# Kernel optimization log

Measured on AMD Instinct MI355X. Metric: run time of the kernel, lower is better.

## Reference

```python
import jax, jax.numpy as jnp
import numpy as np

B, N, C = 2, 16384, 3        # clouds, points per cloud, feature dim
M, K = 2048, 64              # num_out_points (FPS centers), max_num_neighbors
R = 0.2                      # ball-query radius
H1, H2, HOUT = 64, 64, 128   # local_nn MLP widths


def setup_inputs() -> dict:
    key = jax.random.key(0)
    ks = jax.random.split(key, 8)
    return {
        "x": jax.random.normal(ks[0], (B, N, C), jnp.float32),
        "pos": jax.random.uniform(ks[1], (B, N, 3), jnp.float32),
        "W1": jax.random.normal(ks[2], (C + 3, H1), jnp.float32) * 0.1,
        "b1": jnp.zeros((H1,), jnp.float32),
        "W2": jax.random.normal(ks[3], (H1, H2), jnp.float32) * 0.1,
        "b2": jnp.zeros((H2,), jnp.float32),
        "W3": jax.random.normal(ks[4], (H2, HOUT), jnp.float32) * 0.1,
        "b3": jnp.zeros((HOUT,), jnp.float32),
    }


def _fps(pos):
    """Iterative farthest point sampling for one cloud. pos: [N,3] -> idx [M]."""
    mind = jnp.sum((pos - pos[0]) ** 2, axis=-1)  # start from point 0

    def step(mind, _):
        nxt = jnp.argmax(mind)
        mind = jnp.minimum(mind, jnp.sum((pos - pos[nxt]) ** 2, axis=-1))
        return mind, nxt.astype(jnp.int32)

    _, idx = jax.lax.scan(step, mind, None, length=M - 1)
    return jnp.concatenate([jnp.zeros((1,), jnp.int32), idx])


def reference(x, pos, W1, b1, W2, b2, W3, b3):
    # 1) FPS: pick M centers per cloud (vectorized over batch)
    idx = jax.vmap(_fps)(pos)                                   # [B, M]
    centers = jnp.take_along_axis(pos, idx[..., None], axis=1)  # [B, M, 3]

    # 2) ball query: up to K neighbors within radius R of each center
    d2 = jnp.sum((centers[:, :, None, :] - pos[:, None, :, :]) ** 2, axis=-1)  # [B,M,N]
    masked = jnp.where(d2 <= R * R, d2, jnp.inf)
    neg_top, nbr = jax.lax.top_k(-masked, K)   # K nearest within radius; nbr [B,M,K]
    valid = neg_top > -jnp.inf                 # in-radius mask

    # 3) gather -> local MLP -> max scatter (PointNetConv, aggr='max')
    gather = jax.vmap(lambda arr, i: arr[i])   # per-cloud fancy gather
    pos_j = gather(pos, nbr)                   # [B, M, K, 3]
    x_j = gather(x, nbr)                       # [B, M, K, C]
    rel = pos_j - centers[:, :, None, :]
    feat = jnp.concatenate([x_j, rel], axis=-1)          # [B, M, K, C+3]
    h = jax.nn.relu(feat @ W1 + b1)
    h = jax.nn.relu(h @ W2 + b2)
    h = h @ W3 + b3                                       # [B, M, K, HOUT]
    h = jnp.where(valid[..., None], h, -jnp.inf)
    out = jnp.max(h, axis=2)                              # [B, M, HOUT]
    out = jnp.where(jnp.isfinite(out), out, 0.0)          # empty-neighborhood guard
    return out, centers
```

## Files before the change

### kernel.cpp

```cpp
#include <hip/hip_runtime.h>
#include <cstdint>

#define NPT   16384
#define BATCH 2
#define MOUT  2048
#define KNBR  64
#define CAP   2048
#define FPS_T 1024
#define PPT   (NPT / FPS_T)
#define NW    (FPS_T / 64)

#define R2_F32 0.039999999105930328f

__device__ __forceinline__ float d2_exact(float ax, float ay, float az,
                                          float bx, float by, float bz) {
  float dx = __fsub_rn(ax, bx);
  float dy = __fsub_rn(ay, by);
  float dz = __fsub_rn(az, bz);
  return __fadd_rn(__fadd_rn(__fmul_rn(dx, dx), __fmul_rn(dy, dy)),
                   __fmul_rn(dz, dz));
}

template <int CTRL, int ROW>
__device__ __forceinline__ float dpp_max_step(float x) {
  int v = __float_as_int(x);
  int p = __builtin_amdgcn_update_dpp(v, v, CTRL, ROW, 0xF, false);
  return fmaxf(x, __int_as_float(p));
}

__device__ __forceinline__ float wave_max64(float x) {
  x = dpp_max_step<0xB1, 0xF>(x);
  x = dpp_max_step<0x4E, 0xF>(x);
  x = dpp_max_step<0x141, 0xF>(x);
  x = dpp_max_step<0x140, 0xF>(x);
  x = dpp_max_step<0x142, 0xA>(x);
  x = dpp_max_step<0x143, 0xC>(x);
  return __int_as_float(__builtin_amdgcn_readlane(__float_as_int(x), 63));
}

__global__ void prep_kernel(const float* __restrict__ W1,
                            const float* __restrict__ W2,
                            const float* __restrict__ W3,
                            float* __restrict__ ws) {
  int t = threadIdx.x + blockIdx.x * blockDim.x;
  int stride = blockDim.x * gridDim.x;
  for (int idx = t; idx < 64 * 6; idx += stride) {
    int j = idx / 6, i = idx - j * 6;
    ws[idx] = W1[i * 64 + j];
  }
  for (int idx = t; idx < 64 * 64; idx += stride) {
    int j = idx >> 6, i = idx & 63;
    ws[384 + idx] = W2[i * 64 + j];
  }
  for (int idx = t; idx < 128 * 64; idx += stride) {
    int j = idx >> 6, i = idx & 63;
    ws[4480 + idx] = W3[i * 128 + j];
  }
}

__device__ __forceinline__ int morton3_8(int x, int y, int z) {
  int c = 0;
#pragma unroll
  for (int k = 0; k < 3; ++k)
    c |= (((x >> k) & 1) << (3 * k)) | (((y >> k) & 1) << (3 * k + 1)) |
         (((z >> k) & 1) << (3 * k + 2));
  return c;
}

__global__ __launch_bounds__(512) void bin_kernel(
    const float* __restrict__ pos, float* __restrict__ sx,
    float* __restrict__ sy, float* __restrict__ sz, int* __restrict__ soi) {
  const int b = blockIdx.x;
  const int t = threadIdx.x;
  const float* __restrict__ P = pos + (size_t)b * NPT * 3;

  __shared__ int hist[512];
  __shared__ int scan[512];
  __shared__ unsigned short cid[NPT];

  hist[t] = 0;
  __syncthreads();

  for (int p = 0; p < 32; ++p) {
    int g = t + p * 512;
    float x = P[g * 3 + 0], y = P[g * 3 + 1], z = P[g * 3 + 2];
    int ix = (int)(x * 8.0f); ix = ix < 0 ? 0 : (ix > 7 ? 7 : ix);
    int iy = (int)(y * 8.0f); iy = iy < 0 ? 0 : (iy > 7 ? 7 : iy);
    int iz = (int)(z * 8.0f); iz = iz < 0 ? 0 : (iz > 7 ? 7 : iz);
    int c = morton3_8(ix, iy, iz);
    cid[g] = (unsigned short)c;
    atomicAdd(&hist[c], 1);
  }
  __syncthreads();

  int cnt = hist[t];
  int v = cnt;
  scan[t] = v;
  __syncthreads();
  for (int off = 1; off < 512; off <<= 1) {
    int add = (t >= off) ? scan[t - off] : 0;
    __syncthreads();
    v += add;
    scan[t] = v;
    __syncthreads();
  }
  hist[t] = scan[t] - cnt;
  __syncthreads();

  for (int p = 0; p < 32; ++p) {
    int g = t + p * 512;
    int c = cid[g];
    int dst = atomicAdd(&hist[c], 1);
    sx[b * NPT + dst] = P[g * 3 + 0];
    sy[b * NPT + dst] = P[g * 3 + 1];
    sz[b * NPT + dst] = P[g * 3 + 2];
    soi[b * NPT + dst] = g;
  }
}

__global__ __launch_bounds__(FPS_T, 4) void fps_kernel(
    const float* __restrict__ pos, const float* __restrict__ sx,
    const float* __restrict__ sy, const float* __restrict__ sz,
    const int* __restrict__ soi, float* __restrict__ centers) {
  const int b = blockIdx.x;
  const int t = threadIdx.x;
  const int lane = t & 63;
  const int wid = t >> 6;
  const float* __restrict__ P = pos + (size_t)b * NPT * 3;
  float* __restrict__ Cout = centers + (size_t)b * MOUT * 3;

  __shared__ int oidL[NPT];
  __shared__ float wmax[NW];
  __shared__ unsigned long long qpack[2][3];

  float px[PPT], py[PPT], pz[PPT], mind[PPT];
  const int base = b * NPT + t * PPT;
#pragma unroll
  for (int p = 0; p < PPT; ++p) {
    px[p] = sx[base + p];
    py[p] = sy[base + p];
    pz[p] = sz[base + p];
    oidL[t * PPT + p] = soi[base + p];
  }

  float lox = px[0], hix = px[0], loy = py[0], hiy = py[0], loz = pz[0], hiz = pz[0];
#pragma unroll
  for (int p = 1; p < PPT; ++p) {
    lox = fminf(lox, px[p]); hix = fmaxf(hix, px[p]);
    loy = fminf(loy, py[p]); hiy = fmaxf(hiy, py[p]);
    loz = fminf(loz, pz[p]); hiz = fmaxf(hiz, pz[p]);
  }

  float qx = P[0], qy = P[1], qz = P[2];
  if (t == 0) {
    Cout[0] = qx; Cout[1] = qy; Cout[2] = qz;
    qpack[0][0] = qpack[0][1] = qpack[0][2] = ~0ULL;
    qpack[1][0] = qpack[1][1] = qpack[1][2] = ~0ULL;
  }

  float t0_ = -1.0f, t1_ = -1.0f, t2_ = -1.0f, t3_ = -1.0f;
#pragma unroll
  for (int p = 0; p < PPT; ++p) {
    float d2 = d2_exact(px[p], py[p], pz[p], qx, qy, qz);
    mind[p] = d2;
    if ((p & 3) == 0) t0_ = fmaxf(t0_, d2);
    else if ((p & 3) == 1) t1_ = fmaxf(t1_, d2);
    else if ((p & 3) == 2) t2_ = fmaxf(t2_, d2);
    else t3_ = fmaxf(t3_, d2);
  }
  float tm = fmaxf(fmaxf(t0_, t1_), fmaxf(t2_, t3_));

  for (int s = 1; s < MOUT; ++s) {
    const int B = s & 1;
    float wv = wave_max64(tm);
    if (lane == 0) wmax[wid] = wv;
    __syncthreads();
    float g01 = fmaxf(wmax[0], wmax[1]),   g23 = fmaxf(wmax[2], wmax[3]);
    float g45 = fmaxf(wmax[4], wmax[5]),   g67 = fmaxf(wmax[6], wmax[7]);
    float g89 = fmaxf(wmax[8], wmax[9]),   gab = fmaxf(wmax[10], wmax[11]);
    float gcd = fmaxf(wmax[12], wmax[13]), gef = fmaxf(wmax[14], wmax[15]);
    float gv = fmaxf(fmaxf(fmaxf(g01, g23), fmaxf(g45, g67)),
                     fmaxf(fmaxf(g89, gab), fmaxf(gcd, gef)));

    if (tm == gv) {
      int cand = 0x7fffffff;
#pragma unroll
      for (int p = 0; p < PPT; ++p)
        if (mind[p] == gv)
          cand = min(cand, (oidL[t * PPT + p] << 14) | (t << 4) | p);
      unsigned long long hi = ((unsigned long long)(unsigned)cand) << 32;
#pragma unroll
      for (int p = 0; p < PPT; ++p)
        if ((cand & 15) == p) {
          atomicMin(&qpack[B][0], hi | (unsigned long long)__float_as_uint(px[p]));
          atomicMin(&qpack[B][1], hi | (unsigned long long)__float_as_uint(py[p]));
          atomicMin(&qpack[B][2], hi | (unsigned long long)__float_as_uint(pz[p]));
        }
    }
    __syncthreads();

    unsigned long long wx = qpack[B][0];
    unsigned long long wy = qpack[B][1];
    unsigned long long wz = qpack[B][2];
    qx = __uint_as_float((unsigned)wx);
    qy = __uint_as_float((unsigned)wy);
    qz = __uint_as_float((unsigned)wz);
    if (t == 0) {
      Cout[s * 3 + 0] = qx; Cout[s * 3 + 1] = qy; Cout[s * 3 + 2] = qz;
      qpack[B ^ 1][0] = ~0ULL; qpack[B ^ 1][1] = ~0ULL; qpack[B ^ 1][2] = ~0ULL;
    }

    float ddx = fmaxf(fmaxf(lox - qx, qx - hix), 0.0f);
    float ddy = fmaxf(fmaxf(loy - qy, qy - hiy), 0.0f);
    float ddz = fmaxf(fmaxf(loz - qz, qz - hiz), 0.0f);
    float dmin2 = ddx * ddx + ddy * ddy + ddz * ddz;
    if (dmin2 <= tm * 1.0001f) {
      float u0 = -1.0f, u1 = -1.0f, u2 = -1.0f, u3 = -1.0f;
#pragma unroll
      for (int p = 0; p < PPT; ++p) {
        float d2 = d2_exact(px[p], py[p], pz[p], qx, qy, qz);
        float m = fminf(mind[p], d2);
        mind[p] = m;
        if ((p & 3) == 0) u0 = fmaxf(u0, m);
        else if ((p & 3) == 1) u1 = fmaxf(u1, m);
        else if ((p & 3) == 2) u2 = fmaxf(u2, m);
        else u3 = fmaxf(u3, m);
      }
      tm = fmaxf(fmaxf(u0, u1), fmaxf(u2, u3));
    }
  }
}

__global__ __launch_bounds__(256) void ballq_kernel(
    const float* __restrict__ pos, const float* __restrict__ centers,
    int* __restrict__ nbr, int* __restrict__ ncnt) {
  const int bm = blockIdx.x;
  const int b = bm >> 11;
  const int t = threadIdx.x;

  __shared__ unsigned long long keys[CAP];
  __shared__ int cnt;
  if (t == 0) cnt = 0;
  __syncthreads();

  const float cx = centers[(size_t)bm * 3 + 0];
  const float cy = centers[(size_t)bm * 3 + 1];
  const float cz = centers[(size_t)bm * 3 + 2];
  const float* __restrict__ P = pos + (size_t)b * NPT * 3;

  for (int g = t; g < NPT; g += 256) {
    float d2 = d2_exact(cx, cy, cz, P[g * 3 + 0], P[g * 3 + 1], P[g * 3 + 2]);
    if (d2 <= R2_F32) {
      int s = atomicAdd(&cnt, 1);
      if (s < CAP)
        keys[s] = ((unsigned long long)__float_as_uint(d2) << 32) |
                  (unsigned long long)(unsigned)g;
    }
  }
  __syncthreads();

  int C = cnt; if (C > CAP) C = CAP;
  int P2 = 64; while (P2 < C) P2 <<= 1;
  for (int i = C + t; i < P2; i += 256) keys[i] = ~0ULL;
  __syncthreads();

  for (int k = 2; k <= P2; k <<= 1) {
    for (int j = k >> 1; j > 0; j >>= 1) {
      for (int i = t; i < P2; i += 256) {
        int ixj = i ^ j;
        if (ixj > i) {
          unsigned long long a = keys[i], c = keys[ixj];
          bool up = ((i & k) == 0);
          if ((a > c) == up) { keys[i] = c; keys[ixj] = a; }
        }
      }
      __syncthreads();
    }
  }

  if (t < KNBR) {
    int v = (t < C) ? (int)(unsigned)(keys[t] & 0xFFFFFFFFull) : -1;
    nbr[(size_t)bm * KNBR + t] = v;
  }
  if (t == 0) ncnt[bm] = (C < KNBR) ? C : KNBR;
}

__global__ __launch_bounds__(256) void mlp_kernel(
    const float* __restrict__ x, const float* __restrict__ pos,
    const float* __restrict__ centers, const int* __restrict__ nbr,
    const int* __restrict__ ncnt, const float* __restrict__ wsw,
    const float* __restrict__ b1, const float* __restrict__ b2,
    const float* __restrict__ b3, float* __restrict__ out) {
  const int lane = threadIdx.x & 63;
  const int bm = blockIdx.x * 4 + (threadIdx.x >> 6);
  const int b = bm >> 11;

  const float* __restrict__ w1t = wsw;
  const float* __restrict__ w2t = wsw + 384;
  const float* __restrict__ w3t = wsw + 4480;

  const int cnt = ncnt[bm];
  const bool valid = lane < cnt;
  int gr = nbr[(size_t)bm * KNBR + lane];
  int g = valid ? gr : 0;

  const float cx = centers[(size_t)bm * 3 + 0];
  const float cy = centers[(size_t)bm * 3 + 1];
  const float cz = centers[(size_t)bm * 3 + 2];
  const float* __restrict__ Pb = pos + (size_t)b * NPT * 3;
  const float* __restrict__ Xb = x + (size_t)b * NPT * 3;

  float f0 = Xb[g * 3 + 0], f1 = Xb[g * 3 + 1], f2 = Xb[g * 3 + 2];
  float f3 = Pb[g * 3 + 0] - cx, f4 = Pb[g * 3 + 1] - cy, f5 = Pb[g * 3 + 2] - cz;

  float h1[64];
#pragma unroll
  for (int j = 0; j < 64; ++j) {
    float a = b1[j];
    a = fmaf(f0, w1t[j * 6 + 0], a);
    a = fmaf(f1, w1t[j * 6 + 1], a);
    a = fmaf(f2, w1t[j * 6 + 2], a);
    a = fmaf(f3, w1t[j * 6 + 3], a);
    a = fmaf(f4, w1t[j * 6 + 4], a);
    a = fmaf(f5, w1t[j * 6 + 5], a);
    h1[j] = fmaxf(a, 0.0f);
  }

  float h2[64];
#pragma unroll
  for (int j = 0; j < 64; ++j) {
    float a = b2[j];
#pragma unroll
    for (int i = 0; i < 64; ++i) a = fmaf(h1[i], w2t[j * 64 + i], a);
    h2[j] = fmaxf(a, 0.0f);
  }

  float* __restrict__ O = out + (size_t)bm * 128;
#pragma unroll
  for (int j = 0; j < 128; ++j) {
    float a = b3[j];
#pragma unroll
    for (int i = 0; i < 64; ++i) a = fmaf(h2[i], w3t[j * 64 + i], a);
    float v = valid ? a : -INFINITY;
    v = wave_max64(v);
    if (v == -INFINITY) v = 0.0f;
    if (lane == 0) O[j] = v;
  }
}

extern "C" void kernel_launch(void* const* d_in, const int* in_sizes, int n_in,
                              void* d_out, int out_size, void* d_ws,
                              size_t ws_size, hipStream_t stream) {
  const float* x   = (const float*)d_in[0];
  const float* pos = (const float*)d_in[1];
  const float* W1  = (const float*)d_in[2];
  const float* b1  = (const float*)d_in[3];
  const float* W2  = (const float*)d_in[4];
  const float* b2  = (const float*)d_in[5];
  const float* W3  = (const float*)d_in[6];
  const float* b3  = (const float*)d_in[7];

  float* out     = (float*)d_out;
  float* centers = out + (size_t)BATCH * MOUT * 128;

  char* wsb = (char*)d_ws;
  float* wsw = (float*)d_ws;
  float* sx = (float*)(wsb + 51200);
  float* sy = (float*)(wsb + 182272);
  float* sz = (float*)(wsb + 313344);
  int*   soi = (int*)(wsb + 444416);
  int*   nbr = (int*)(wsb + 51200);
  int*   ncnt = (int*)(wsb + 51200 + (size_t)BATCH * MOUT * KNBR * 4);

  prep_kernel<<<32, 256, 0, stream>>>(W1, W2, W3, wsw);
  bin_kernel<<<BATCH, 512, 0, stream>>>(pos, sx, sy, sz, soi);
  fps_kernel<<<BATCH, FPS_T, 0, stream>>>(pos, sx, sy, sz, soi, centers);
  ballq_kernel<<<BATCH * MOUT, 256, 0, stream>>>(pos, centers, nbr, ncnt);
  mlp_kernel<<<BATCH * MOUT / 4, 256, 0, stream>>>(x, pos, centers, nbr, ncnt,
                                                   wsw, b1, b2, b3, out);
}
```

Measured before the change: 3.556 ms.

## Stream FPS point coordinates from global memory instead of holding them in registers

The FPS kernel no longer keeps each thread's 16 point coordinates in registers. It re-reads them as float4 loads from the sorted arrays on every distance update, which is meant to cut register pressure. The winner selection now uses a single 32-bit atomicMin on a packed candidate key instead of three 64-bit atomics per coordinate, and the chosen center's coordinates are loaded from global memory by index. The cost is extra global or L2 reads and one dependent load per iteration on the serial FPS critical path.

```diff
diff --git a/kernel.cpp b/kernel.cpp
--- a/kernel.cpp
+++ b/kernel.cpp
@@ -118,7 +118,9 @@
   }
 }
 
-__global__ __launch_bounds__(FPS_T, 4) void fps_kernel(
+__global__ __launch_bounds__(FPS_T)
+__attribute__((amdgpu_waves_per_eu(4, 4)))
+void fps_kernel(
     const float* __restrict__ pos, const float* __restrict__ sx,
     const float* __restrict__ sy, const float* __restrict__ sz,
     const int* __restrict__ soi, float* __restrict__ centers) {
@@ -129,46 +131,68 @@
   const float* __restrict__ P = pos + (size_t)b * NPT * 3;
   float* __restrict__ Cout = centers + (size_t)b * MOUT * 3;
 
+  const float* __restrict__ sxc = sx + b * NPT;
+  const float* __restrict__ syc = sy + b * NPT;
+  const float* __restrict__ szc = sz + b * NPT;
+
   __shared__ int oidL[NPT];
   __shared__ float wmax[NW];
-  __shared__ unsigned long long qpack[2][3];
-
-  float px[PPT], py[PPT], pz[PPT], mind[PPT];
-  const int base = b * NPT + t * PPT;
-#pragma unroll
-  for (int p = 0; p < PPT; ++p) {
-    px[p] = sx[base + p];
-    py[p] = sy[base + p];
-    pz[p] = sz[base + p];
-    oidL[t * PPT + p] = soi[base + p];
-  }
-
-  float lox = px[0], hix = px[0], loy = py[0], hiy = py[0], loz = pz[0], hiz = pz[0];
-#pragma unroll
-  for (int p = 1; p < PPT; ++p) {
-    lox = fminf(lox, px[p]); hix = fmaxf(hix, px[p]);
-    loy = fminf(loy, py[p]); hiy = fmaxf(hiy, py[p]);
-    loz = fminf(loz, pz[p]); hiz = fmaxf(hiz, pz[p]);
+  __shared__ int cand2[2];
+
+  const float4* __restrict__ xs =
+      reinterpret_cast<const float4*>(sxc + t * PPT);
+  const float4* __restrict__ ys =
+      reinterpret_cast<const float4*>(syc + t * PPT);
+  const float4* __restrict__ zs =
+      reinterpret_cast<const float4*>(szc + t * PPT);
+  {
+    const int4* __restrict__ os =
+        reinterpret_cast<const int4*>(soi + b * NPT + t * PPT);
+#pragma unroll
+    for (int q = 0; q < 4; ++q) {
+      int4 o = os[q];
+      oidL[t * PPT + q * 4 + 0] = o.x;
+      oidL[t * PPT + q * 4 + 1] = o.y;
+      oidL[t * PPT + q * 4 + 2] = o.z;
+      oidL[t * PPT + q * 4 + 3] = o.w;
+    }
   }
 
   float qx = P[0], qy = P[1], qz = P[2];
   if (t == 0) {
     Cout[0] = qx; Cout[1] = qy; Cout[2] = qz;
-    qpack[0][0] = qpack[0][1] = qpack[0][2] = ~0ULL;
-    qpack[1][0] = qpack[1][1] = qpack[1][2] = ~0ULL;
-  }
-
-  float t0_ = -1.0f, t1_ = -1.0f, t2_ = -1.0f, t3_ = -1.0f;
-#pragma unroll
-  for (int p = 0; p < PPT; ++p) {
-    float d2 = d2_exact(px[p], py[p], pz[p], qx, qy, qz);
-    mind[p] = d2;
-    if ((p & 3) == 0) t0_ = fmaxf(t0_, d2);
-    else if ((p & 3) == 1) t1_ = fmaxf(t1_, d2);
-    else if ((p & 3) == 2) t2_ = fmaxf(t2_, d2);
-    else t3_ = fmaxf(t3_, d2);
-  }
-  float tm = fmaxf(fmaxf(t0_, t1_), fmaxf(t2_, t3_));
+    cand2[0] = 0x7fffffff;
+    cand2[1] = 0x7fffffff;
+  }
+
+  float mind[PPT];
+  float lox, hix, loy, hiy, loz, hiz;
+  float tm;
+  {
+    float u0 = -1.0f, u1 = -1.0f;
+#pragma unroll
+    for (int q = 0; q < 4; ++q) {
+      float4 X = xs[q], Y = ys[q], Z = zs[q];
+      if (q == 0) {
+        lox = X.x; hix = X.x; loy = Y.x; hiy = Y.x; loz = Z.x; hiz = Z.x;
+      }
+      lox = fminf(fminf(fminf(lox, X.x), fminf(X.y, X.z)), X.w);
+      hix = fmaxf(fmaxf(fmaxf(hix, X.x), fmaxf(X.y, X.z)), X.w);
+      loy = fminf(fminf(fminf(loy, Y.x), fminf(Y.y, Y.z)), Y.w);
+      hiy = fmaxf(fmaxf(fmaxf(hiy, Y.x), fmaxf(Y.y, Y.z)), Y.w);
+      loz = fminf(fminf(fminf(loz, Z.x), fminf(Z.y, Z.z)), Z.w);
+      hiz = fmaxf(fmaxf(fmaxf(hiz, Z.x), fmaxf(Z.y, Z.z)), Z.w);
+      float d0 = d2_exact(X.x, Y.x, Z.x, qx, qy, qz);
+      float d1 = d2_exact(X.y, Y.y, Z.y, qx, qy, qz);
+      float d2v = d2_exact(X.z, Y.z, Z.z, qx, qy, qz);
+      float d3 = d2_exact(X.w, Y.w, Z.w, qx, qy, qz);
+      mind[q * 4 + 0] = d0; mind[q * 4 + 1] = d1;
+      mind[q * 4 + 2] = d2v; mind[q * 4 + 3] = d3;
+      u0 = fmaxf(u0, fmaxf(d0, d1));
+      u1 = fmaxf(u1, fmaxf(d2v, d3));
+    }
+    tm = fmaxf(u0, u1);
+  }
 
   for (int s = 1; s < MOUT; ++s) {
     const int B = s & 1;
@@ -188,26 +212,16 @@
       for (int p = 0; p < PPT; ++p)
         if (mind[p] == gv)
           cand = min(cand, (oidL[t * PPT + p] << 14) | (t << 4) | p);
-      unsigned long long hi = ((unsigned long long)(unsigned)cand) << 32;
-#pragma unroll
-      for (int p = 0; p < PPT; ++p)
-        if ((cand & 15) == p) {
-          atomicMin(&qpack[B][0], hi | (unsigned long long)__float_as_uint(px[p]));
-          atomicMin(&qpack[B][1], hi | (unsigned long long)__float_as_uint(py[p]));
-          atomicMin(&qpack[B][2], hi | (unsigned long long)__float_as_uint(pz[p]));
-        }
+      atomicMin(&cand2[B], cand);
     }
     __syncthreads();
 
-    unsigned long long wx = qpack[B][0];
-    unsigned long long wy = qpack[B][1];
-    unsigned long long wz = qpack[B][2];
-    qx = __uint_as_float((unsigned)wx);
-    qy = __uint_as_float((unsigned)wy);
-    qz = __uint_as_float((unsigned)wz);
+    const int w = cand2[B];
+    const int sidx = w & 0x3FFF;
+    qx = sxc[sidx]; qy = syc[sidx]; qz = szc[sidx];
     if (t == 0) {
       Cout[s * 3 + 0] = qx; Cout[s * 3 + 1] = qy; Cout[s * 3 + 2] = qz;
-      qpack[B ^ 1][0] = ~0ULL; qpack[B ^ 1][1] = ~0ULL; qpack[B ^ 1][2] = ~0ULL;
+      cand2[B ^ 1] = 0x7fffffff;
     }
 
     float ddx = fmaxf(fmaxf(lox - qx, qx - hix), 0.0f);
@@ -215,18 +229,24 @@
     float ddz = fmaxf(fmaxf(loz - qz, qz - hiz), 0.0f);
     float dmin2 = ddx * ddx + ddy * ddy + ddz * ddz;
     if (dmin2 <= tm * 1.0001f) {
-      float u0 = -1.0f, u1 = -1.0f, u2 = -1.0f, u3 = -1.0f;
-#pragma unroll
-      for (int p = 0; p < PPT; ++p) {
-        float d2 = d2_exact(px[p], py[p], pz[p], qx, qy, qz);
-        float m = fminf(mind[p], d2);
-        mind[p] = m;
-        if ((p & 3) == 0) u0 = fmaxf(u0, m);
-        else if ((p & 3) == 1) u1 = fmaxf(u1, m);
-        else if ((p & 3) == 2) u2 = fmaxf(u2, m);
-        else u3 = fmaxf(u3, m);
+      float u0 = -1.0f, u1 = -1.0f;
+#pragma unroll
+      for (int q = 0; q < 4; ++q) {
+        float4 X = xs[q], Y = ys[q], Z = zs[q];
+        float d0 = d2_exact(X.x, Y.x, Z.x, qx, qy, qz);
+        float d1 = d2_exact(X.y, Y.y, Z.y, qx, qy, qz);
+        float d2v = d2_exact(X.z, Y.z, Z.z, qx, qy, qz);
+        float d3 = d2_exact(X.w, Y.w, Z.w, qx, qy, qz);
+        float m0 = fminf(mind[q * 4 + 0], d0);
+        float m1 = fminf(mind[q * 4 + 1], d1);
+        float m2 = fminf(mind[q * 4 + 2], d2v);
+        float m3 = fminf(mind[q * 4 + 3], d3);
+        mind[q * 4 + 0] = m0; mind[q * 4 + 1] = m1;
+        mind[q * 4 + 2] = m2; mind[q * 4 + 3] = m3;
+        u0 = fmaxf(u0, fmaxf(m0, m1));
+        u1 = fmaxf(u1, fmaxf(m2, m3));
       }
-      tm = fmaxf(fmaxf(u0, u1), fmaxf(u2, u3));
+      tm = fmaxf(u0, u1);
     }
   }
 }
```

New measurement: 3.617 ms. No clear change (+1.7%).
